# Kernel optimization log

Hardware: AMD Instinct MI355X
Metric: run time of the kernel (lower is better)

The kernel has to match this reference:

```python
import jax, jax.numpy as jnp
import numpy as np

NUM_NODES = 50000
NUM_EDGES = 800000
NUM_GRAPHS = 256
FEAT = 128
STATE = 64
ROUNDS = 4
M = 32


def setup_inputs() -> dict:
    key = jax.random.key(0)
    ks = jax.random.split(key, 12)
    x = jax.random.normal(ks[0], (NUM_NODES, FEAT), dtype=jnp.float32)
    edge_index = jax.random.randint(ks[1], (2, NUM_EDGES), 0, NUM_NODES, dtype=jnp.int64)
    batch = jnp.sort(jax.random.randint(ks[2], (NUM_NODES,), 0, NUM_GRAPHS, dtype=jnp.int64))
    s = 0.1  # weight init scale
    return {
        "x": x,
        "edge_index": edge_index,
        "batch": batch,
        "in_W": jax.random.normal(ks[3], (FEAT, STATE), dtype=jnp.float32) * s,
        "in_b": jnp.zeros((STATE,), dtype=jnp.float32),
        "msg_W": jax.random.normal(ks[4], (ROUNDS, STATE, STATE), dtype=jnp.float32) * s,
        "msg_b": jnp.zeros((ROUNDS, STATE), dtype=jnp.float32),
        "upd_W": jax.random.normal(ks[5], (ROUNDS, STATE, STATE), dtype=jnp.float32) * s,
        "upd_b": jnp.zeros((ROUNDS, STATE), dtype=jnp.float32),
        "mean_W": jax.random.normal(ks[6], (STATE, M), dtype=jnp.float32) * s,
        "mean_b": jnp.zeros((M,), dtype=jnp.float32),
        "logvar_W": jax.random.normal(ks[7], (STATE, M), dtype=jnp.float32) * s,
        "logvar_b": jnp.zeros((M,), dtype=jnp.float32),
    }


def reference(x, edge_index, batch, in_W, in_b, msg_W, msg_b, upd_W, upd_b,
              mean_W, mean_b, logvar_W, logvar_b):
    num_nodes = x.shape[0]
    src, dst = edge_index[0], edge_index[1]  # (to, from) -> gather src, scatter dst
    # input net (dropout is identity in eval mode)
    state = jax.nn.relu(x @ in_W + in_b)  # [N, S]
    for r in range(ROUNDS):
        message = jax.nn.relu(state @ msg_W[r] + msg_b[r])          # [N, S]
        gathered = message[src]                                       # [E, S] irregular gather
        aggregated = jax.ops.segment_sum(gathered, dst, num_segments=num_nodes)  # [N, S] scatter-add
        state = state + jax.nn.relu(aggregated @ upd_W[r] + upd_b[r])
    graph_state = jax.ops.segment_sum(state, batch, num_segments=NUM_GRAPHS)  # [G, S]
    mean = graph_state @ mean_W + mean_b                              # [G, M]
    log_var = jnp.clip(graph_state @ logvar_W + logvar_b, -20.0, 2.0)
    std = jnp.exp(0.5 * log_var)
    return jnp.stack([mean, std])  # [2, G, M] -> Normal(mean, std) params
```

## Files before the change

kernel.cpp:

```cpp
#include <hip/hip_runtime.h>
#include <math.h>

#define NODES  50000
#define EDGES  800000
#define GRAPHS 256
#define FEAT   128
#define STATE  64
#define M_OUT  32
#define ROUNDS 4
#define NT32   ((NODES + 31) / 32)
#define HALF   32
#define PLANE  (50000L * 32L)
#define CAP    64
#define OVFMAX 8192
#define NFILL  391
#define NFT    (NFILL * 256)

typedef unsigned short bfraw;

__device__ __forceinline__ bfraw f2bf(float f) {
    union { float f; unsigned int i; } v; v.f = f;
    unsigned int r = v.i + 0x7FFF + ((v.i >> 16) & 1);
    return (bfraw)(r >> 16);
}
__device__ __forceinline__ int packbf(float lo, float hi) {
    return ((int)f2bf(hi) << 16) | (int)f2bf(lo);
}
__device__ __forceinline__ void addv8(float* acc, int4 v, float m) {
    union { int i; float f; } t;
    t.i = v.x << 16;                  acc[0] += t.f * m;
    t.i = v.x & (int)0xffff0000;      acc[1] += t.f * m;
    t.i = v.y << 16;                  acc[2] += t.f * m;
    t.i = v.y & (int)0xffff0000;      acc[3] += t.f * m;
    t.i = v.z << 16;                  acc[4] += t.f * m;
    t.i = v.z & (int)0xffff0000;      acc[5] += t.f * m;
    t.i = v.w << 16;                  acc[6] += t.f * m;
    t.i = v.w & (int)0xffff0000;      acc[7] += t.f * m;
}
__device__ __forceinline__ int4 pack8(const float* a) {
    int4 o;
    o.x = packbf(a[0], a[1]); o.y = packbf(a[2], a[3]);
    o.z = packbf(a[4], a[5]); o.w = packbf(a[6], a[7]);
    return o;
}

__device__ __forceinline__ void gather_to_lds(
    const int* __restrict__ cnt, const unsigned short* __restrict__ csr,
    const int* __restrict__ ovfc, const int* __restrict__ ovf,
    const bfraw* __restrict__ plane0, const bfraw* __restrict__ plane1,
    float* __restrict__ sa)
{
    float dummy = 0.f;
    {
        const bfraw* p = (threadIdx.x < 128) ? plane0 : plane1;
        long s = (long)blockIdx.x * 1024 + (long)(threadIdx.x & 127) * 8;
        if (s + 8 <= PLANE) {
            int4 a = *(const int4*)(p + s);
            union { int i; float f; } t; t.i = a.x << 16;
            dummy = t.f;
        }
    }

    const int row = threadIdx.x >> 3;
    const int q   = (threadIdx.x & 7) * 8;
    const int n   = blockIdx.x * 32 + row;
    const bfraw* plane = (q < HALF) ? plane0 : plane1;
    const int qq = (q < HALF) ? q : q - HALF;

    int cn = (n < NODES) ? cnt[n] : 0;
    if (cn > CAP) cn = CAP;
    const unsigned short* crow = csr + (long)n * CAP;

    float acc[8] = {0.f, 0.f, 0.f, 0.f, 0.f, 0.f, 0.f, 0.f};
    for (int i = 0; i < cn; i += 8) {
        int4 ia = *(const int4*)(crow + i);
        int rem = cn - i;
        int idx[8];
        idx[0] = ia.x & 0xffff; idx[1] = ((unsigned)ia.x) >> 16;
        idx[2] = ia.y & 0xffff; idx[3] = ((unsigned)ia.y) >> 16;
        idx[4] = ia.z & 0xffff; idx[5] = ((unsigned)ia.z) >> 16;
        idx[6] = ia.w & 0xffff; idx[7] = ((unsigned)ia.w) >> 16;
        int4 v[8];
        #pragma unroll
        for (int j = 0; j < 8; j++) {
            int s_ = (j < rem) ? idx[j] : idx[0];
            v[j] = *(const int4*)(plane + (long)s_ * HALF + qq);
        }
        #pragma unroll
        for (int j = 0; j < 8; j++) addv8(acc, v[j], (j < rem) ? 1.f : 0.f);
    }
    acc[0] += dummy * 0.0f;

    int oc = *ovfc;
    if (oc > 0) {
        if (oc > OVFMAX) oc = OVFMAX;
        for (int t = 0; t < oc; t++) {
            int pk = ovf[t];
            if ((pk >> 16) == n) {
                int4 v = *(const int4*)(plane + (long)(pk & 0xffff) * HALF + qq);
                addv8(acc, v, 1.f);
            }
        }
    }

    *(float4*)(sa + row * 68 + q)     = make_float4(acc[0], acc[1], acc[2], acc[3]);
    *(float4*)(sa + row * 68 + q + 4) = make_float4(acc[4], acc[5], acc[6], acc[7]);
}

__global__ __launch_bounds__(256) void k_in_msg(
    const int* __restrict__ ei, int* __restrict__ cnt,
    unsigned short* __restrict__ csr, int* __restrict__ ovfc, int* __restrict__ ovf,
    const float* __restrict__ x, const float* __restrict__ inW, const float* __restrict__ inb,
    const float* __restrict__ msgW, const float* __restrict__ msgb,
    float* __restrict__ state, bfraw* __restrict__ msg0, bfraw* __restrict__ msg1)
{
    __shared__ float sW[64 * STATE];
    __shared__ float sB[32 * 68];
    __shared__ float sInb[STATE], sMsgb[STATE];

    if (blockIdx.x < NFILL) {
        const int t = blockIdx.x * 256 + threadIdx.x;
        int src[8], dst[8];
        #pragma unroll
        for (int k = 0; k < 8; k++) {
            int e = t + k * NFT;
            bool v = (e < EDGES);
            src[k] = v ? __builtin_nontemporal_load(ei + e) : 0;
            dst[k] = v ? __builtin_nontemporal_load(ei + EDGES + e) : -1;
        }
        int slot[8];
        #pragma unroll
        for (int k = 0; k < 8; k++)
            slot[k] = (dst[k] >= 0) ? atomicAdd(&cnt[dst[k]], 1) : 0;
        #pragma unroll
        for (int k = 0; k < 8; k++) {
            if (dst[k] < 0) continue;
            if (slot[k] < CAP) csr[(long)dst[k] * CAP + slot[k]] = (unsigned short)src[k];
            else { int o = atomicAdd(ovfc, 1); if (o < OVFMAX) ovf[o] = (dst[k] << 16) | src[k]; }
        }
        return;
    }

    const int bx  = blockIdx.x - NFILL;
    const int row = threadIdx.x >> 3;
    const int q8  = (threadIdx.x & 7) << 3;
    const int base = bx * 32;
    const int n = base + row;

    if (threadIdx.x < STATE) {
        sInb[threadIdx.x]  = inb[threadIdx.x];
        sMsgb[threadIdx.x] = msgb[threadIdx.x];
    }
    for (int i = threadIdx.x; i < 512; i += 256) {
        int r = i >> 4, q = (i & 15) << 2;
        float4 v = make_float4(0.f, 0.f, 0.f, 0.f);
        if (base + r < NODES) v = *(const float4*)(x + (long)(base + r) * FEAT + q);
        *(float4*)(sB + r * 68 + q) = v;
    }
    for (int i = threadIdx.x; i < 1024; i += 256)
        *(float4*)(sW + i * 4) = *(const float4*)(inW + i * 4);
    __syncthreads();

    float a[8];
    #pragma unroll
    for (int j = 0; j < 8; j++) a[j] = sInb[q8 + j];
    const float* xr = sB + row * 68;
    #pragma unroll 8
    for (int k = 0; k < 64; k++) {
        float xv = xr[k];
        float4 w0 = *(const float4*)(sW + k * STATE + q8);
        float4 w1 = *(const float4*)(sW + k * STATE + q8 + 4);
        a[0] += xv * w0.x; a[1] += xv * w0.y; a[2] += xv * w0.z; a[3] += xv * w0.w;
        a[4] += xv * w1.x; a[5] += xv * w1.y; a[6] += xv * w1.z; a[7] += xv * w1.w;
    }
    __syncthreads();
    for (int i = threadIdx.x; i < 512; i += 256) {
        int r = i >> 4, q = (i & 15) << 2;
        float4 v = make_float4(0.f, 0.f, 0.f, 0.f);
        if (base + r < NODES) v = *(const float4*)(x + (long)(base + r) * FEAT + 64 + q);
        *(float4*)(sB + r * 68 + q) = v;
    }
    for (int i = threadIdx.x; i < 1024; i += 256)
        *(float4*)(sW + i * 4) = *(const float4*)(inW + 64 * STATE + i * 4);
    __syncthreads();
    #pragma unroll 8
    for (int k = 0; k < 64; k++) {
        float xv = xr[k];
        float4 w0 = *(const float4*)(sW + k * STATE + q8);
        float4 w1 = *(const float4*)(sW + k * STATE + q8 + 4);
        a[0] += xv * w0.x; a[1] += xv * w0.y; a[2] += xv * w0.z; a[3] += xv * w0.w;
        a[4] += xv * w1.x; a[5] += xv * w1.y; a[6] += xv * w1.z; a[7] += xv * w1.w;
    }
    #pragma unroll
    for (int j = 0; j < 8; j++) a[j] = fmaxf(a[j], 0.f);
    if (n < NODES) {
        *(float4*)(state + (long)n * STATE + q8)     = make_float4(a[0], a[1], a[2], a[3]);
        *(float4*)(state + (long)n * STATE + q8 + 4) = make_float4(a[4], a[5], a[6], a[7]);
    }
    __syncthreads();
    *(float4*)(sB + row * 68 + q8)     = make_float4(a[0], a[1], a[2], a[3]);
    *(float4*)(sB + row * 68 + q8 + 4) = make_float4(a[4], a[5], a[6], a[7]);
    for (int i = threadIdx.x; i < 1024; i += 256)
        *(float4*)(sW + i * 4) = *(const float4*)(msgW + i * 4);
    __syncthreads();

    float m[8];
    #pragma unroll
    for (int j = 0; j < 8; j++) m[j] = sMsgb[q8 + j];
    const float* sr = sB + row * 68;
    #pragma unroll 8
    for (int k = 0; k < STATE; k++) {
        float sv = sr[k];
        float4 w0 = *(const float4*)(sW + k * STATE + q8);
        float4 w1 = *(const float4*)(sW + k * STATE + q8 + 4);
        m[0] += sv * w0.x; m[1] += sv * w0.y; m[2] += sv * w0.z; m[3] += sv * w0.w;
        m[4] += sv * w1.x; m[5] += sv * w1.y; m[6] += sv * w1.z; m[7] += sv * w1.w;
    }
    #pragma unroll
    for (int j = 0; j < 8; j++) m[j] = fmaxf(m[j], 0.f);
    if (n < NODES) {
        bfraw* dst = (q8 < HALF) ? (msg0 + (long)n * HALF + q8) : (msg1 + (long)n * HALF + (q8 - HALF));
        *(int4*)dst = pack8(m);
    }
}

__global__ __launch_bounds__(256) void k_round_msg(
    const int* __restrict__ cnt, const unsigned short* __restrict__ csr,
    const int* __restrict__ ovfc, const int* __restrict__ ovf,
    const bfraw* __restrict__ plane0, const bfraw* __restrict__ plane1,
    const float* __restrict__ updW, const float* __restrict__ updb,
    const float* __restrict__ msgW, const float* __restrict__ msgb,
    float* __restrict__ state, bfraw* __restrict__ msg0, bfraw* __restrict__ msg1)
{
    __shared__ float sW[64 * STATE];
    __shared__ float sUpdb[STATE], sMsgb[STATE];
    __shared__ float sa[32 * 68];

    const int row = threadIdx.x >> 3;
    const int q8  = (threadIdx.x & 7) << 3;
    const int n = blockIdx.x * 32 + row;

    if (threadIdx.x < STATE) {
        sUpdb[threadIdx.x] = updb[threadIdx.x];
        sMsgb[threadIdx.x] = msgb[threadIdx.x];
    }
    for (int i = threadIdx.x; i < 1024; i += 256)
        *(float4*)(sW + i * 4) = *(const float4*)(updW + i * 4);

    gather_to_lds(cnt, csr, ovfc, ovf, plane0, plane1, sa);
    __syncthreads();

    float a[8];
    #pragma unroll
    for (int j = 0; j < 8; j++) a[j] = sUpdb[q8 + j];
    const float* ar = sa + row * 68;
    #pragma unroll 8
    for (int k = 0; k < STATE; k++) {
        float av = ar[k];
        float4 w0 = *(const float4*)(sW + k * STATE + q8);
        float4 w1 = *(const float4*)(sW + k * STATE + q8 + 4);
        a[0] += av * w0.x; a[1] += av * w0.y; a[2] += av * w0.z; a[3] += av * w0.w;
        a[4] += av * w1.x; a[5] += av * w1.y; a[6] += av * w1.z; a[7] += av * w1.w;
    }
    #pragma unroll
    for (int j = 0; j < 8; j++) a[j] = fmaxf(a[j], 0.f);
    float s[8] = {0.f,0.f,0.f,0.f,0.f,0.f,0.f,0.f};
    if (n < NODES) {
        float4 st0 = *(const float4*)(state + (long)n * STATE + q8);
        float4 st1 = *(const float4*)(state + (long)n * STATE + q8 + 4);
        s[0] = st0.x + a[0]; s[1] = st0.y + a[1]; s[2] = st0.z + a[2]; s[3] = st0.w + a[3];
        s[4] = st1.x + a[4]; s[5] = st1.y + a[5]; s[6] = st1.z + a[6]; s[7] = st1.w + a[7];
        *(float4*)(state + (long)n * STATE + q8)     = make_float4(s[0], s[1], s[2], s[3]);
        *(float4*)(state + (long)n * STATE + q8 + 4) = make_float4(s[4], s[5], s[6], s[7]);
    }
    __syncthreads();
    *(float4*)(sa + row * 68 + q8)     = make_float4(s[0], s[1], s[2], s[3]);
    *(float4*)(sa + row * 68 + q8 + 4) = make_float4(s[4], s[5], s[6], s[7]);
    for (int i = threadIdx.x; i < 1024; i += 256)
        *(float4*)(sW + i * 4) = *(const float4*)(msgW + i * 4);
    __syncthreads();

    float m[8];
    #pragma unroll
    for (int j = 0; j < 8; j++) m[j] = sMsgb[q8 + j];
    const float* sr = sa + row * 68;
    #pragma unroll 8
    for (int k = 0; k < STATE; k++) {
        float sv = sr[k];
        float4 w0 = *(const float4*)(sW + k * STATE + q8);
        float4 w1 = *(const float4*)(sW + k * STATE + q8 + 4);
        m[0] += sv * w0.x; m[1] += sv * w0.y; m[2] += sv * w0.z; m[3] += sv * w0.w;
        m[4] += sv * w1.x; m[5] += sv * w1.y; m[6] += sv * w1.z; m[7] += sv * w1.w;
    }
    #pragma unroll
    for (int j = 0; j < 8; j++) m[j] = fmaxf(m[j], 0.f);
    if (n < NODES) {
        bfraw* dst = (q8 < HALF) ? (msg0 + (long)n * HALF + q8) : (msg1 + (long)n * HALF + (q8 - HALF));
        *(int4*)dst = pack8(m);
    }
}

__global__ __launch_bounds__(256) void k_round_pool(
    const int* __restrict__ cnt, const unsigned short* __restrict__ csr,
    const int* __restrict__ ovfc, const int* __restrict__ ovf,
    const bfraw* __restrict__ plane0, const bfraw* __restrict__ plane1,
    const float* __restrict__ updW, const float* __restrict__ updb,
    const float* __restrict__ state, const int* __restrict__ batch,
    float* __restrict__ gs)
{
    __shared__ float sW[64 * STATE];
    __shared__ float sUpdb[STATE];
    __shared__ float sa[32 * 68];
    __shared__ int   sg[32];

    const int row = threadIdx.x >> 3;
    const int q8  = (threadIdx.x & 7) << 3;
    const int base = blockIdx.x * 32;
    const int n = base + row;

    if (threadIdx.x < STATE) sUpdb[threadIdx.x] = updb[threadIdx.x];
    for (int i = threadIdx.x; i < 1024; i += 256)
        *(float4*)(sW + i * 4) = *(const float4*)(updW + i * 4);
    if (threadIdx.x < 32) {
        int nn = base + threadIdx.x;
        sg[threadIdx.x] = batch[nn < NODES ? nn : NODES - 1];
    }

    gather_to_lds(cnt, csr, ovfc, ovf, plane0, plane1, sa);
    __syncthreads();

    float a[8];
    #pragma unroll
    for (int j = 0; j < 8; j++) a[j] = sUpdb[q8 + j];
    const float* ar = sa + row * 68;
    #pragma unroll 8
    for (int k = 0; k < STATE; k++) {
        float av = ar[k];
        float4 w0 = *(const float4*)(sW + k * STATE + q8);
        float4 w1 = *(const float4*)(sW + k * STATE + q8 + 4);
        a[0] += av * w0.x; a[1] += av * w0.y; a[2] += av * w0.z; a[3] += av * w0.w;
        a[4] += av * w1.x; a[5] += av * w1.y; a[6] += av * w1.z; a[7] += av * w1.w;
    }
    float s[8] = {0.f,0.f,0.f,0.f,0.f,0.f,0.f,0.f};
    if (n < NODES) {
        float4 st0 = *(const float4*)(state + (long)n * STATE + q8);
        float4 st1 = *(const float4*)(state + (long)n * STATE + q8 + 4);
        s[0] = st0.x + fmaxf(a[0], 0.f); s[1] = st0.y + fmaxf(a[1], 0.f);
        s[2] = st0.z + fmaxf(a[2], 0.f); s[3] = st0.w + fmaxf(a[3], 0.f);
        s[4] = st1.x + fmaxf(a[4], 0.f); s[5] = st1.y + fmaxf(a[5], 0.f);
        s[6] = st1.z + fmaxf(a[6], 0.f); s[7] = st1.w + fmaxf(a[7], 0.f);
    }
    __syncthreads();
    *(float4*)(sa + row * 68 + q8)     = make_float4(s[0], s[1], s[2], s[3]);
    *(float4*)(sa + row * 68 + q8 + 4) = make_float4(s[4], s[5], s[6], s[7]);
    __syncthreads();

    if (threadIdx.x < STATE) {
        const int f = threadIdx.x;
        float run = sa[f];
        int g = sg[0];
        #pragma unroll
        for (int r = 1; r < 32; r++) {
            int g2 = sg[r];
            float v = sa[r * 68 + f];
            if (g2 != g) {
                atomicAdd(&gs[g * STATE + f], run);
                run = v; g = g2;
            } else {
                run += v;
            }
        }
        atomicAdd(&gs[g * STATE + f], run);
    }
}

__global__ __launch_bounds__(64) void k_final(
    const float* __restrict__ gs,
    const float* __restrict__ meanW, const float* __restrict__ meanb,
    const float* __restrict__ lvW, const float* __restrict__ lvb,
    float* __restrict__ out)
{
    __shared__ float row[STATE];
    const int g = blockIdx.x;
    const int j = threadIdx.x;
    row[j] = gs[g * STATE + j];
    __syncthreads();
    if (j < M_OUT) {
        float acc = meanb[j];
        #pragma unroll
        for (int k = 0; k < STATE; k++) acc += row[k] * meanW[k * M_OUT + j];
        out[g * M_OUT + j] = acc;
    } else {
        int jj = j - M_OUT;
        float acc = lvb[jj];
        #pragma unroll
        for (int k = 0; k < STATE; k++) acc += row[k] * lvW[k * M_OUT + jj];
        acc = fminf(fmaxf(acc, -20.f), 2.f);
        out[GRAPHS * M_OUT + g * M_OUT + jj] = expf(0.5f * acc);
    }
}

extern "C" void kernel_launch(void* const* d_in, const int* in_sizes, int n_in,
                              void* d_out, int out_size, void* d_ws, size_t ws_size,
                              hipStream_t stream) {
    const float* x     = (const float*)d_in[0];
    const int*   ei    = (const int*)d_in[1];
    const int*   batch = (const int*)d_in[2];
    const float* inW   = (const float*)d_in[3];
    const float* inb   = (const float*)d_in[4];
    const float* msgW  = (const float*)d_in[5];
    const float* msgb  = (const float*)d_in[6];
    const float* updW  = (const float*)d_in[7];
    const float* updb  = (const float*)d_in[8];
    const float* meanW = (const float*)d_in[9];
    const float* meanb = (const float*)d_in[10];
    const float* lvW   = (const float*)d_in[11];
    const float* lvb   = (const float*)d_in[12];
    float* out = (float*)d_out;

    const size_t NS   = (size_t)NODES * STATE * sizeof(float);
    const size_t PLB  = (size_t)PLANE * sizeof(bfraw);
    char* ws = (char*)d_ws;
    size_t off = 0;
    auto alloc = [&](size_t bytes) { void* p = ws + off; off += (bytes + 255) & ~(size_t)255; return p; };
    float* state  = (float*)alloc(NS);
    bfraw* msgA0  = (bfraw*)alloc(PLB);
    bfraw* msgA1  = (bfraw*)alloc(PLB);
    bfraw* msgB0  = (bfraw*)alloc(PLB);
    bfraw* msgB1  = (bfraw*)alloc(PLB);
    float* gs     = (float*)alloc((size_t)GRAPHS * STATE * sizeof(float));
    int*   cnt    = (int*)alloc((size_t)NODES * sizeof(int));
    int*   ovfc   = (int*)alloc(256);
    int*   ovf    = (int*)alloc((size_t)OVFMAX * sizeof(int));
    unsigned short* csr = (unsigned short*)alloc((size_t)NODES * CAP * sizeof(unsigned short));

    hipMemsetAsync(cnt, 0, (size_t)NODES * sizeof(int), stream);
    hipMemsetAsync(ovfc, 0, sizeof(int), stream);
    hipMemsetAsync(gs, 0, (size_t)GRAPHS * STATE * sizeof(float), stream);

    k_in_msg<<<NFILL + NT32, 256, 0, stream>>>(ei, cnt, csr, ovfc, ovf,
                                               x, inW, inb, msgW, msgb, state, msgA0, msgA1);

    bfraw *mi0 = msgA0, *mi1 = msgA1, *mo0 = msgB0, *mo1 = msgB1;
    for (int r = 0; r < ROUNDS; r++) {
        if (r < ROUNDS - 1) {
            k_round_msg<<<NT32, 256, 0, stream>>>(
                cnt, csr, ovfc, ovf, mi0, mi1,
                updW + r * STATE * STATE, updb + r * STATE,
                msgW + (r + 1) * STATE * STATE, msgb + (r + 1) * STATE,
                state, mo0, mo1);
            bfraw* t0 = mi0; mi0 = mo0; mo0 = t0;
            bfraw* t1 = mi1; mi1 = mo1; mo1 = t1;
        } else {
            k_round_pool<<<NT32, 256, 0, stream>>>(
                cnt, csr, ovfc, ovf, mi0, mi1,
                updW + r * STATE * STATE, updb + r * STATE,
                state, batch, gs);
        }
    }

    k_final<<<GRAPHS, 64, 0, stream>>>(gs, meanW, meanb, lvW, lvb, out);
}
```

Before: 302.2 us.

## Use single interleaved bf16 message buffer and split CSR fill into own kernel

Replaces the two half-width bf16 message planes (32 features each) with one contiguous 64-feature row per node, so each gathered neighbor row is a single 128-byte span instead of two 64-byte pieces in separate arrays. The CSR fill work, previously fused into the input/message kernel via extra blocks with 8 edges per thread, moves to a separate one-edge-per-thread kernel launched first. This trades locality in the neighbor gather and simpler addressing for an extra kernel launch and the loss of overlap between the CSR fill and the input projection.

```diff
diff --git a/kernel.cpp b/kernel.cpp
--- a/kernel.cpp
+++ b/kernel.cpp
@@ -9,12 +9,8 @@
 #define M_OUT  32
 #define ROUNDS 4
 #define NT32   ((NODES + 31) / 32)
-#define HALF   32
-#define PLANE  (50000L * 32L)
 #define CAP    64
 #define OVFMAX 8192
-#define NFILL  391
-#define NFT    (NFILL * 256)
 
 typedef unsigned short bfraw;
 
@@ -44,18 +40,29 @@
     return o;
 }
 
+__global__ __launch_bounds__(256) void k_fill(
+    const int* __restrict__ ei, int* __restrict__ cnt,
+    unsigned short* __restrict__ csr, int* __restrict__ ovfc, int* __restrict__ ovf)
+{
+    int e = blockIdx.x * 256 + threadIdx.x;
+    if (e >= EDGES) return;
+    int src = __builtin_nontemporal_load(ei + e);
+    int dst = __builtin_nontemporal_load(ei + EDGES + e);
+    int slot = atomicAdd(&cnt[dst], 1);
+    if (slot < CAP) csr[(long)dst * CAP + slot] = (unsigned short)src;
+    else { int o = atomicAdd(ovfc, 1); if (o < OVFMAX) ovf[o] = (dst << 16) | src; }
+}
+
 __device__ __forceinline__ void gather_to_lds(
     const int* __restrict__ cnt, const unsigned short* __restrict__ csr,
     const int* __restrict__ ovfc, const int* __restrict__ ovf,
-    const bfraw* __restrict__ plane0, const bfraw* __restrict__ plane1,
-    float* __restrict__ sa)
+    const bfraw* __restrict__ msg, float* __restrict__ sa)
 {
     float dummy = 0.f;
     {
-        const bfraw* p = (threadIdx.x < 128) ? plane0 : plane1;
-        long s = (long)blockIdx.x * 1024 + (long)(threadIdx.x & 127) * 8;
-        if (s + 8 <= PLANE) {
-            int4 a = *(const int4*)(p + s);
+        long s = (long)blockIdx.x * 2048 + (long)threadIdx.x * 8;
+        if (s + 8 <= (long)NODES * STATE) {
+            int4 a = *(const int4*)(msg + s);
             union { int i; float f; } t; t.i = a.x << 16;
             dummy = t.f;
         }
@@ -64,8 +71,6 @@
     const int row = threadIdx.x >> 3;
     const int q   = (threadIdx.x & 7) * 8;
     const int n   = blockIdx.x * 32 + row;
-    const bfraw* plane = (q < HALF) ? plane0 : plane1;
-    const int qq = (q < HALF) ? q : q - HALF;
 
     int cn = (n < NODES) ? cnt[n] : 0;
     if (cn > CAP) cn = CAP;
@@ -84,7 +89,7 @@
         #pragma unroll
         for (int j = 0; j < 8; j++) {
             int s_ = (j < rem) ? idx[j] : idx[0];
-            v[j] = *(const int4*)(plane + (long)s_ * HALF + qq);
+            v[j] = *(const int4*)(msg + (long)s_ * STATE + q);
         }
         #pragma unroll
         for (int j = 0; j < 8; j++) addv8(acc, v[j], (j < rem) ? 1.f : 0.f);
@@ -97,7 +102,7 @@
         for (int t = 0; t < oc; t++) {
             int pk = ovf[t];
             if ((pk >> 16) == n) {
-                int4 v = *(const int4*)(plane + (long)(pk & 0xffff) * HALF + qq);
+                int4 v = *(const int4*)(msg + (long)(pk & 0xffff) * STATE + q);
                 addv8(acc, v, 1.f);
             }
         }
@@ -108,43 +113,17 @@
 }
 
 __global__ __launch_bounds__(256) void k_in_msg(
-    const int* __restrict__ ei, int* __restrict__ cnt,
-    unsigned short* __restrict__ csr, int* __restrict__ ovfc, int* __restrict__ ovf,
     const float* __restrict__ x, const float* __restrict__ inW, const float* __restrict__ inb,
     const float* __restrict__ msgW, const float* __restrict__ msgb,
-    float* __restrict__ state, bfraw* __restrict__ msg0, bfraw* __restrict__ msg1)
+    float* __restrict__ state, bfraw* __restrict__ msg)
 {
     __shared__ float sW[64 * STATE];
     __shared__ float sB[32 * 68];
     __shared__ float sInb[STATE], sMsgb[STATE];
 
-    if (blockIdx.x < NFILL) {
-        const int t = blockIdx.x * 256 + threadIdx.x;
-        int src[8], dst[8];
-        #pragma unroll
-        for (int k = 0; k < 8; k++) {
-            int e = t + k * NFT;
-            bool v = (e < EDGES);
-            src[k] = v ? __builtin_nontemporal_load(ei + e) : 0;
-            dst[k] = v ? __builtin_nontemporal_load(ei + EDGES + e) : -1;
-        }
-        int slot[8];
-        #pragma unroll
-        for (int k = 0; k < 8; k++)
-            slot[k] = (dst[k] >= 0) ? atomicAdd(&cnt[dst[k]], 1) : 0;
-        #pragma unroll
-        for (int k = 0; k < 8; k++) {
-            if (dst[k] < 0) continue;
-            if (slot[k] < CAP) csr[(long)dst[k] * CAP + slot[k]] = (unsigned short)src[k];
-            else { int o = atomicAdd(ovfc, 1); if (o < OVFMAX) ovf[o] = (dst[k] << 16) | src[k]; }
-        }
-        return;
-    }
-
-    const int bx  = blockIdx.x - NFILL;
     const int row = threadIdx.x >> 3;
     const int q8  = (threadIdx.x & 7) << 3;
-    const int base = bx * 32;
+    const int base = blockIdx.x * 32;
     const int n = base + row;
 
     if (threadIdx.x < STATE) {
@@ -218,19 +197,17 @@
     }
     #pragma unroll
     for (int j = 0; j < 8; j++) m[j] = fmaxf(m[j], 0.f);
-    if (n < NODES) {
-        bfraw* dst = (q8 < HALF) ? (msg0 + (long)n * HALF + q8) : (msg1 + (long)n * HALF + (q8 - HALF));
-        *(int4*)dst = pack8(m);
-    }
+    if (n < NODES)
+        *(int4*)(msg + (long)n * STATE + q8) = pack8(m);
 }
 
 __global__ __launch_bounds__(256) void k_round_msg(
     const int* __restrict__ cnt, const unsigned short* __restrict__ csr,
     const int* __restrict__ ovfc, const int* __restrict__ ovf,
-    const bfraw* __restrict__ plane0, const bfraw* __restrict__ plane1,
+    const bfraw* __restrict__ msg_in,
     const float* __restrict__ updW, const float* __restrict__ updb,
     const float* __restrict__ msgW, const float* __restrict__ msgb,
-    float* __restrict__ state, bfraw* __restrict__ msg0, bfraw* __restrict__ msg1)
+    float* __restrict__ state, bfraw* __restrict__ msg_out)
 {
     __shared__ float sW[64 * STATE];
     __shared__ float sUpdb[STATE], sMsgb[STATE];
@@ -247,7 +224,7 @@
     for (int i = threadIdx.x; i < 1024; i += 256)
         *(float4*)(sW + i * 4) = *(const float4*)(updW + i * 4);
 
-    gather_to_lds(cnt, csr, ovfc, ovf, plane0, plane1, sa);
+    gather_to_lds(cnt, csr, ovfc, ovf, msg_in, sa);
     __syncthreads();
 
     float a[8];
@@ -294,16 +271,14 @@
     }
     #pragma unroll
     for (int j = 0; j < 8; j++) m[j] = fmaxf(m[j], 0.f);
-    if (n < NODES) {
-        bfraw* dst = (q8 < HALF) ? (msg0 + (long)n * HALF + q8) : (msg1 + (long)n * HALF + (q8 - HALF));
-        *(int4*)dst = pack8(m);
-    }
+    if (n < NODES)
+        *(int4*)(msg_out + (long)n * STATE + q8) = pack8(m);
 }
 
 __global__ __launch_bounds__(256) void k_round_pool(
     const int* __restrict__ cnt, const unsigned short* __restrict__ csr,
     const int* __restrict__ ovfc, const int* __restrict__ ovf,
-    const bfraw* __restrict__ plane0, const bfraw* __restrict__ plane1,
+    const bfraw* __restrict__ msg_in,
     const float* __restrict__ updW, const float* __restrict__ updb,
     const float* __restrict__ state, const int* __restrict__ batch,
     float* __restrict__ gs)
@@ -326,7 +301,7 @@
         sg[threadIdx.x] = batch[nn < NODES ? nn : NODES - 1];
     }
 
-    gather_to_lds(cnt, csr, ovfc, ovf, plane0, plane1, sa);
+    gather_to_lds(cnt, csr, ovfc, ovf, msg_in, sa);
     __syncthreads();
 
     float a[8];
@@ -419,15 +394,13 @@
     float* out = (float*)d_out;
 
     const size_t NS   = (size_t)NODES * STATE * sizeof(float);
-    const size_t PLB  = (size_t)PLANE * sizeof(bfraw);
+    const size_t MSGB = (size_t)NODES * STATE * sizeof(bfraw);
     char* ws = (char*)d_ws;
     size_t off = 0;
     auto alloc = [&](size_t bytes) { void* p = ws + off; off += (bytes + 255) & ~(size_t)255; return p; };
     float* state  = (float*)alloc(NS);
-    bfraw* msgA0  = (bfraw*)alloc(PLB);
-    bfraw* msgA1  = (bfraw*)alloc(PLB);
-    bfraw* msgB0  = (bfraw*)alloc(PLB);
-    bfraw* msgB1  = (bfraw*)alloc(PLB);
+    bfraw* msgA   = (bfraw*)alloc(MSGB);
+    bfraw* msgB   = (bfraw*)alloc(MSGB);
     float* gs     = (float*)alloc((size_t)GRAPHS * STATE * sizeof(float));
     int*   cnt    = (int*)alloc((size_t)NODES * sizeof(int));
     int*   ovfc   = (int*)alloc(256);
@@ -438,22 +411,21 @@
     hipMemsetAsync(ovfc, 0, sizeof(int), stream);
     hipMemsetAsync(gs, 0, (size_t)GRAPHS * STATE * sizeof(float), stream);
 
-    k_in_msg<<<NFILL + NT32, 256, 0, stream>>>(ei, cnt, csr, ovfc, ovf,
-                                               x, inW, inb, msgW, msgb, state, msgA0, msgA1);
-
-    bfraw *mi0 = msgA0, *mi1 = msgA1, *mo0 = msgB0, *mo1 = msgB1;
+    k_fill<<<(EDGES + 255) / 256, 256, 0, stream>>>(ei, cnt, csr, ovfc, ovf);
+    k_in_msg<<<NT32, 256, 0, stream>>>(x, inW, inb, msgW, msgb, state, msgA);
+
+    bfraw *mi = msgA, *mo = msgB;
     for (int r = 0; r < ROUNDS; r++) {
         if (r < ROUNDS - 1) {
             k_round_msg<<<NT32, 256, 0, stream>>>(
-                cnt, csr, ovfc, ovf, mi0, mi1,
+                cnt, csr, ovfc, ovf, mi,
                 updW + r * STATE * STATE, updb + r * STATE,
                 msgW + (r + 1) * STATE * STATE, msgb + (r + 1) * STATE,
-                state, mo0, mo1);
-            bfraw* t0 = mi0; mi0 = mo0; mo0 = t0;
-            bfraw* t1 = mi1; mi1 = mo1; mo1 = t1;
+                state, mo);
+            bfraw* t = mi; mi = mo; mo = t;
         } else {
             k_round_pool<<<NT32, 256, 0, stream>>>(
-                cnt, csr, ovfc, ovf, mi0, mi1,
+                cnt, csr, ovfc, ovf, mi,
                 updW + r * STATE * STATE, updb + r * STATE,
                 state, batch, gs);
         }
```

Measured after the change: 309.3 us. 1.02x slower.
